# Kernel tuning notes

Measured on AMD Instinct MI355X. Metric: run time of the kernel, lower is better.

Reference implementation:

```python
import jax, jax.numpy as jnp
import numpy as np

L, H, D_IN, D_OUT = 2, 768, 768, 512


def _gru_layer(x, w_ih, w_hh, b_ih, b_hh):
    # x: [B,T,D]; w_ih: [3H,D]; w_hh: [3H,H]; b_ih,b_hh: [3H]
    # PyTorch GRU gate order: r, z, n
    gates_x = jnp.einsum('btd,gd->btg', x, w_ih) + b_ih  # [B,T,3H], precomputed once
    gates_x = jnp.swapaxes(gates_x, 0, 1)  # [T,B,3H] for scan over time
    h0 = jnp.zeros((x.shape[0], w_hh.shape[1]), dtype=x.dtype)

    def step(h, gx):
        gh = h @ w_hh.T + b_hh  # [B,3H]
        xr, xz, xn = jnp.split(gx, 3, axis=-1)
        hr, hz, hn = jnp.split(gh, 3, axis=-1)
        r = jax.nn.sigmoid(xr + hr)
        z = jax.nn.sigmoid(xz + hz)
        n = jnp.tanh(xn + r * hn)
        h_new = (1.0 - z) * n + z * h
        return h_new, h_new

    _, ys = jax.lax.scan(step, h0, gates_x)  # ys: [T,B,H]
    return jnp.swapaxes(ys, 0, 1)  # [B,T,H]


def setup_inputs() -> dict:
    key = jax.random.key(0)
    ks = jax.random.split(key, 6)
    B, T = 16, 1024
    s = 1.0 / np.sqrt(H)  # PyTorch RNN init scale
    x = jax.random.normal(ks[0], (B, T, D_IN), dtype=jnp.float32)
    # stacked per-layer GRU weights (D_IN == H so layer 0 stacks cleanly)
    w_ih = jax.random.uniform(ks[1], (L, 3 * H, H), minval=-s, maxval=s, dtype=jnp.float32)
    w_hh = jax.random.uniform(ks[2], (L, 3 * H, H), minval=-s, maxval=s, dtype=jnp.float32)
    b_ih = jax.random.uniform(ks[3], (L, 3 * H), minval=-s, maxval=s, dtype=jnp.float32)
    b_hh = jax.random.uniform(ks[4], (L, 3 * H), minval=-s, maxval=s, dtype=jnp.float32)
    w_fc = jax.random.normal(ks[5], (D_OUT, H), dtype=jnp.float32) * 0.02
    b_fc = jnp.zeros((D_OUT,), dtype=jnp.float32)
    return {"x": x, "w_ih": w_ih, "w_hh": w_hh, "b_ih": b_ih, "b_hh": b_hh,
            "w_fc": w_fc, "b_fc": b_fc}


def reference(x, w_ih, w_hh, b_ih, b_hh, w_fc, b_fc):
    out = x
    for l in range(L):  # small fixed layer loop
        out = _gru_layer(out, w_ih[l], w_hh[l], b_ih[l], b_hh[l])
    out = jnp.einsum('bth,oh->bto', out, w_fc) + b_fc  # Linear(768->512)
    return jax.nn.gelu(out, approximate=False)  # torch gelu (exact)
```

## Files before the change

### kernel.cpp

```cpp
#include <hip/hip_runtime.h>
#include <hip/hip_bf16.h>

#define H     768
#define G3    2304
#define BATCH 16
#define TLEN  1024
#define DOUT  512
#define SLICE 32
#define WPG   24
#define NSCAN 96
#define NFC   64
#define NWG   160
#define NTHR  384

typedef __attribute__((ext_vector_type(8))) short short8;
typedef __attribute__((ext_vector_type(4))) float f32x4;
typedef __attribute__((ext_vector_type(4))) unsigned int u32x4;

union U8 { short8 s; unsigned u[4]; unsigned long long q[2]; };

__device__ __forceinline__ float b2f(ushort u) {
  union { unsigned int ui; float f; } v; v.ui = ((unsigned int)u) << 16; return v.f;
}
__device__ __forceinline__ ushort f2b(float f) {
  union { float f; unsigned int ui; } v; v.f = f;
  unsigned int u = v.ui;
  return (ushort)((u + 0x7fffu + ((u >> 16) & 1u)) >> 16);
}

__device__ __forceinline__ unsigned long long agent_ld64(const void* p) {
  return __hip_atomic_load((const unsigned long long*)p, __ATOMIC_RELAXED, __HIP_MEMORY_SCOPE_AGENT);
}
__device__ __forceinline__ unsigned agent_ld32(const void* p) {
  return __hip_atomic_load((const unsigned*)p, __ATOMIC_RELAXED, __HIP_MEMORY_SCOPE_AGENT);
}
__device__ __forceinline__ void agent_st32(void* p, unsigned v) {
  __hip_atomic_store((unsigned*)p, v, __ATOMIC_RELAXED, __HIP_MEMORY_SCOPE_AGENT);
}
__device__ __forceinline__ void agent_st64(void* p, unsigned long long v) {
  __hip_atomic_store((unsigned long long*)p, v, __ATOMIC_RELAXED, __HIP_MEMORY_SCOPE_AGENT);
}

__device__ __forceinline__ void ld64B_agent(const void* p, u32x4* r) {
  asm volatile(
    "global_load_dwordx4 %0, %4, off sc0 sc1\n\t"
    "global_load_dwordx4 %1, %4, off offset:16 sc0 sc1\n\t"
    "global_load_dwordx4 %2, %4, off offset:32 sc0 sc1\n\t"
    "global_load_dwordx4 %3, %4, off offset:48 sc0 sc1\n\t"
    "s_waitcnt vmcnt(0)"
    : "=&v"(r[0]), "=&v"(r[1]), "=&v"(r[2]), "=&v"(r[3])
    : "v"(p) : "memory");
}

__device__ __forceinline__ short8 loadA8(const void* base, bool bf, size_t eidx) {
  if (bf) return *(const short8*)((const ushort*)base + eidx);
  const uint4* f = (const uint4*)((const float*)base + eidx);
  uint4 lo = f[0];
  uint4 hi = f[1];
  U8 r;
  r.u[0] = __builtin_amdgcn_perm(lo.y, lo.x, 0x07060302);
  r.u[1] = __builtin_amdgcn_perm(lo.w, lo.z, 0x07060302);
  r.u[2] = __builtin_amdgcn_perm(hi.y, hi.x, 0x07060302);
  r.u[3] = __builtin_amdgcn_perm(hi.w, hi.z, 0x07060302);
  return r.s;
}
__device__ __forceinline__ short8 loadW8(const void* base, bool bf, size_t eidx) {
  if (bf) return *(const short8*)((const ushort*)base + eidx);
  const float* f = (const float*)base + eidx;
  short8 r;
  #pragma unroll
  for (int i = 0; i < 8; i++) r[i] = (short)f2b(f[i]);
  return r;
}
__device__ __forceinline__ float loadS(const void* p, bool bf, size_t i) {
  return bf ? b2f(((const ushort*)p)[i]) : ((const float*)p)[i];
}

__device__ __forceinline__ bool detect_bf16(const unsigned* xw, int tid, int nthr, int* sh) {
  if (tid == 0) *sh = 0;
  __syncthreads();
  int c = 0;
  for (int i = tid; i < 4096; i += nthr) {
    int e = (int)((xw[i] >> 7) & 0xFF);
    c += (e >= 110 && e <= 140) ? 1 : 0;
  }
  atomicAdd(sh, c);
  __syncthreads();
  return *sh > 2048;
}

__device__ __forceinline__ unsigned* flagp(unsigned* flags, int grp, int wgi, int rep) {
  return flags + (((grp * WPG + wgi) * 4 + rep) * 32);
}

__global__ __launch_bounds__(NTHR) void scan_kernel(
    const void* __restrict__ x,
    const void* __restrict__ w_ih,
    const void* __restrict__ w_hh,
    const void* __restrict__ b_ih,
    const void* __restrict__ b_hh,
    const void* __restrict__ w_fc,
    const void* __restrict__ b_fc,
    unsigned int* flags,
    ushort* h1buf,
    float*  gxbuf1,
    float*  gxbuf2,
    ushort* y2,
    void* __restrict__ out)
{
  const int wg   = blockIdx.x;
  const int tid  = threadIdx.x;
  const int wave = tid >> 6;
  const int lane = tid & 63;
  const int quad = lane >> 4;

  __shared__ ushort h_lds[BATCH * H];
  __shared__ float ghs[96 * 17];
  __shared__ float hold[BATCH * SLICE];
  __shared__ float bih_s[96], bhh_s[96];
  __shared__ unsigned donecnt[2];
  __shared__ int   detsh;

  const bool isbf = detect_bf16((const unsigned*)x, tid, NTHR, &detsh);

  if (wg >= NSCAN) {
    const int fcw = wg - NSCAN;
    const unsigned* fpoll = (wave == 0 && lane < WPG)
        ? flagp(flags, 3, lane, (fcw < 32) ? 2 : 3) : nullptr;
    const int sb  = tid / 24;
    const int seg = tid % 24;
    const int sx  = sb & 7;
    const int ar  = lane & 15;
    const int arx = ar & 7;

    for (int i = 0; i < 16; i++) {
      const int t = fcw + 64 * i;
      if (wave == 0) {
        const int tgt = t + 5;
        for (;;) {
          int v = fpoll ? (int)agent_ld32(fpoll) : 0x7FFFFFFF;
          if (__ballot(v < tgt) == 0ull) break;
          __builtin_amdgcn_s_sleep(8);
        }
      }
      __syncthreads();

      {
        const ushort* src = y2 + ((size_t)sb * TLEN + t) * H + seg * 32;
        u32x4 r4[4];
        ld64B_agent(src, r4);
        #pragma unroll
        for (int j = 0; j < 4; j++)
          *(u32x4*)&h_lds[sb * H + (((seg * 4 + j) ^ sx) * 8)] = r4[j];
      }
      __syncthreads();

      if (wave < 4) {
        const int n0 = wave * 128;
        const ushort* abase = &h_lds[ar * H];
        f32x4 acc[8];
        #pragma unroll
        for (int nt = 0; nt < 8; nt++) acc[nt] = (f32x4){0.f, 0.f, 0.f, 0.f};
        for (int kk = 0; kk < 12; kk++) {
          short8 a0 = *(const short8*)&abase[((quad + 4 * kk) ^ arx) * 8];
          short8 a1 = *(const short8*)&abase[((quad + 4 * (kk + 12)) ^ arx) * 8];
          #pragma unroll
          for (int nt = 0; nt < 8; nt++) {
            const size_t bb = (size_t)(n0 + nt * 16 + ar) * H + quad * 8;
            short8 b0 = loadA8(w_fc, isbf, bb + kk * 32);
            short8 b1 = loadA8(w_fc, isbf, bb + (kk + 12) * 32);
            acc[nt] = __builtin_amdgcn_mfma_f32_16x16x32_bf16(a0, b0, acc[nt], 0, 0, 0);
            acc[nt] = __builtin_amdgcn_mfma_f32_16x16x32_bf16(a1, b1, acc[nt], 0, 0, 0);
          }
        }
        #pragma unroll
        for (int nt = 0; nt < 8; nt++) {
          #pragma unroll
          for (int i2 = 0; i2 < 4; i2++) {
            const int b = quad * 4 + i2;
            const int n = n0 + nt * 16 + ar;
            float v = acc[nt][i2] + loadS(b_fc, isbf, n);
            float g = 0.5f * v * (1.0f + erff(v * 0.70710678118654752f));
            if (isbf) ((ushort*)out)[((size_t)b * TLEN + t) * DOUT + n] = f2b(g);
            else      ((float*)out)[((size_t)b * TLEN + t) * DOUT + n] = g;
          }
        }
      }
      __syncthreads();
    }
    return;
  }

  const int grp  = wg / WPG;
  const int wgi  = wg % WPG;
  const bool isL = (grp == 1 || grp == 3);

  if (tid < 2) donecnt[tid] = 0u;
  for (int i = tid; i < BATCH * SLICE; i += NTHR) hold[i] = 0.0f;

  if (isL) {
    size_t boff = (grp == 3) ? (size_t)G3 : 0;
    for (int gf = tid; gf < 96; gf += NTHR) {
      size_t gidx = boff + (size_t)(gf >> 5) * H + wgi * SLICE + (gf & 31);
      bih_s[gf] = loadS(b_ih, isbf, gidx);
      bhh_s[gf] = loadS(b_hh, isbf, gidx);
    }
  }

  const unsigned* pollp = nullptr;
  int polloff = 0;
  if (wave == 0) {
    if (grp == 0) {
      if (lane == 0) { pollp = flagp(flags, 1, wgi, 2); polloff = -2; }
    } else if (grp == 1) {
      if      (lane == 0)  { pollp = flagp(flags, 0, wgi, 0);       polloff = 0;  }
      else if (lane <= 24) { pollp = flagp(flags, 1, lane - 1, 0);  polloff = 0;  }
      else if (lane <= 48) { pollp = flagp(flags, 2, lane - 25, 0); polloff = -2; }
    } else if (grp == 2) {
      if      (lane < 24)  { pollp = flagp(flags, 1, lane, 1);      polloff = 0;  }
      else if (lane == 24) { pollp = flagp(flags, 3, wgi, 1);       polloff = -1; }
    } else {
      if      (lane == 0)  { pollp = flagp(flags, 2, wgi, 1);       polloff = -1; }
      else if (lane <= 24) { pollp = flagp(flags, 3, lane - 1, 0);  polloff = 0;  }
    }
  }

  const void* Wmat = (grp == 0 || grp == 2) ? w_ih : w_hh;
  const size_t woff = (grp >= 2) ? (size_t)G3 * H : 0;
  const int gate   = wave >> 1;
  const int gfbase = gate * SLICE + (wave & 1) * 16;
  const int nrow   = gate * H + wgi * SLICE + (wave & 1) * 16 + (lane & 15);
  const size_t wbase = woff + (size_t)nrow * H + quad * 8;

  short8 bfrag[24];
  #pragma unroll
  for (int kk = 0; kk < 24; kk++)
    bfrag[kk] = loadW8(Wmat, isbf, wbase + kk * 32);

  const int sb  = tid / 24;
  const int seg = tid % 24;
  const int sx  = sb & 7;

  const int pb = tid >> 4;
  const int pj = (tid & 15) * 2;
  const bool pact = isL && (tid < BATCH * SLICE / 2);

  const int lag = (grp == 1) ? 1 : ((grp == 2) ? 2 : ((grp == 3) ? 4 : 0));

  __syncthreads();

  for (int t = 0; t < TLEN + 4; t++) {
    const int tau = t - lag;
    const bool active = (tau >= 0) && (tau < TLEN);

    if (active) {
      if (wave == 0) {
        for (;;) {
          int v = pollp ? (int)agent_ld32(pollp) : 0x7FFFFFFF;
          if (__ballot(v < t + polloff) == 0ull) break;
          __builtin_amdgcn_s_sleep(1);
        }
      }
      __syncthreads();

      unsigned long long gr01 = 0, gz01 = 0, gn01 = 0;
      if (pact) {
        const float* gxr = ((grp == 1) ? gxbuf1 : gxbuf2)
            + ((size_t)((tau & 3) * WPG + wgi) * BATCH + pb) * 96;
        gr01 = agent_ld64(gxr + pj);
        gz01 = agent_ld64(gxr + 32 + pj);
        gn01 = agent_ld64(gxr + 64 + pj);
      }

      if (grp == 0) {
        const size_t srcbase = ((size_t)sb * TLEN + tau) * H + seg * 32;
        #pragma unroll
        for (int i = 0; i < 4; i++) {
          short8 v = loadA8(x, isbf, srcbase + i * 8);
          *(short8*)&h_lds[sb * H + (((seg * 4 + i) ^ sx) * 8)] = v;
        }
      } else {
        const int hstep = (grp == 3) ? (t - 5) : (t - 2);
        u32x4 r4[4];
        if (hstep >= 0) {
          const ushort* src = (grp == 3)
              ? y2 + ((size_t)sb * TLEN + hstep) * H + seg * 32
              : h1buf + (size_t)(hstep & 3) * (BATCH * H) + (size_t)sb * H + seg * 32;
          ld64B_agent(src, r4);
        } else {
          r4[0] = (u32x4){0u, 0u, 0u, 0u};
          r4[1] = r4[0]; r4[2] = r4[0]; r4[3] = r4[0];
        }
        #pragma unroll
        for (int j = 0; j < 4; j++)
          *(u32x4*)&h_lds[sb * H + (((seg * 4 + j) ^ sx) * 8)] = r4[j];
      }
      __syncthreads();

      const int ar  = lane & 15;
      const int arx = ar & 7;
      const ushort* abase = &h_lds[ar * H];
      f32x4 acc0 = {0.f, 0.f, 0.f, 0.f}, acc1 = {0.f, 0.f, 0.f, 0.f};
      #pragma unroll
      for (int kk = 0; kk < 12; kk++) {
        short8 a0 = *(const short8*)&abase[((quad + 4 * kk) ^ arx) * 8];
        short8 a1 = *(const short8*)&abase[((quad + 4 * (kk + 12)) ^ arx) * 8];
        acc0 = __builtin_amdgcn_mfma_f32_16x16x32_bf16(a0, bfrag[kk],      acc0, 0, 0, 0);
        acc1 = __builtin_amdgcn_mfma_f32_16x16x32_bf16(a1, bfrag[kk + 12], acc1, 0, 0, 0);
      }
      f32x4 acc = acc0 + acc1;

      #pragma unroll
      for (int i = 0; i < 4; i++)
        ghs[(gfbase + ar) * 17 + quad * 4 + i] = acc[i];
      __syncthreads();

      if (!isL) {
        float* gxout = ((grp == 0) ? gxbuf1 : gxbuf2)
            + ((size_t)(tau & 3) * WPG + wgi) * BATCH * 96;
        const int m  = tid / 24;
        const int c4 = (tid % 24) * 4;
        union { unsigned long long q; float f[2]; } p0, p1;
        p0.f[0] = ghs[(c4 + 0) * 17 + m];
        p0.f[1] = ghs[(c4 + 1) * 17 + m];
        p1.f[0] = ghs[(c4 + 2) * 17 + m];
        p1.f[1] = ghs[(c4 + 3) * 17 + m];
        agent_st64(gxout + (size_t)m * 96 + c4,     p0.q);
        agent_st64(gxout + (size_t)m * 96 + c4 + 2, p1.q);
      } else if (pact) {
        union { unsigned long long q; float f[2]; } ur, uz, un;
        ur.q = gr01; uz.q = gz01; un.q = gn01;
        unsigned hpack = 0;
        #pragma unroll
        for (int s = 0; s < 2; s++) {
          const int j = pj + s;
          float rpre = ur.f[s] + bih_s[j]      + ghs[j * 17 + pb]        + bhh_s[j];
          float zpre = uz.f[s] + bih_s[32 + j] + ghs[(32 + j) * 17 + pb] + bhh_s[32 + j];
          float hn   = ghs[(64 + j) * 17 + pb] + bhh_s[64 + j];
          float r = 1.0f / (1.0f + expf(-rpre));
          float z = 1.0f / (1.0f + expf(-zpre));
          float n = tanhf(un.f[s] + bih_s[64 + j] + r * hn);
          float hnew = (1.0f - z) * n + z * hold[pb * SLICE + j];
          hold[pb * SLICE + j] = hnew;
          hpack |= ((unsigned)f2b(hnew)) << (16 * s);
        }
        if (grp == 1)
          agent_st32(h1buf + (size_t)(tau & 3) * (BATCH * H)
                           + (size_t)pb * H + wgi * SLICE + pj, hpack);
        else
          agent_st32(&y2[((size_t)pb * TLEN + tau) * H + wgi * SLICE + pj], hpack);

        asm volatile("s_waitcnt vmcnt(0)" ::: "memory");
        if ((tid & 63) == 0) {
          unsigned prev = atomicAdd(&donecnt[t & 1], 1u);
          if (prev == 3u) {
            donecnt[t & 1] = 0u;
            #pragma unroll
            for (int r = 0; r < 4; r++)
              agent_st32(flagp(flags, grp, wgi, r), (unsigned)(t + 1));
          }
        }
      }
    }

    __syncthreads();
    if (tid < 4 && (!isL || !active))
      agent_st32(flagp(flags, grp, wgi, tid), (unsigned)(t + 1));
  }
}

extern "C" void kernel_launch(void* const* d_in, const int* in_sizes, int n_in,
                              void* d_out, int out_size, void* d_ws, size_t ws_size,
                              hipStream_t stream) {
  const void* x    = d_in[0];
  const void* w_ih = d_in[1];
  const void* w_hh = d_in[2];
  const void* b_ih = d_in[3];
  const void* b_hh = d_in[4];
  const void* w_fc = d_in[5];
  const void* b_fc = d_in[6];

  char* ws = (char*)d_ws;
  unsigned int* flags = (unsigned int*)(ws);
  ushort* h1buf  = (ushort*)(ws + 53248);
  float*  gxbuf1 = (float*)(ws + 151552);
  float*  gxbuf2 = (float*)(ws + 741376);
  ushort* y2     = (ushort*)(ws + 1331200);

  hipMemsetAsync(ws, 0, 49152, stream);
  scan_kernel<<<dim3(NWG), dim3(NTHR), 0, stream>>>(
      x, w_ih, w_hh, b_ih, b_hh, w_fc, b_fc, flags,
      h1buf, gxbuf1, gxbuf2, y2, d_out);
}
```

Baseline: 3.965 ms.

## Co-locate recurrent GRU workgroups on one XCD and sync through local L2

Launches extra workgroups, reads each block's XCC id from a hardware register, and has block 0 assign roles so that each recurrent group's 24 workgroups sit on a single XCD where possible. Those clustered groups exchange hidden state and step flags through XCD-local L2 (sc0 loads, workgroup-scope stores) instead of device-coherent memory, aiming to cut per-timestep synchronization latency on the serial scan. A timeout falls back to the device-coherent path, and the state is still written to global buffers for consumers on other XCDs. This adds a startup rendezvous, relies on placement and cache-coherence assumptions, and spare workgroups exit immediately.

```diff
diff --git a/kernel.cpp b/kernel.cpp
--- a/kernel.cpp
+++ b/kernel.cpp
@@ -8,10 +8,9 @@
 #define DOUT  512
 #define SLICE 32
 #define WPG   24
-#define NSCAN 96
-#define NFC   64
-#define NWG   160
+#define NWG   256
 #define NTHR  384
+#define TMO   4096
 
 typedef __attribute__((ext_vector_type(8))) short short8;
 typedef __attribute__((ext_vector_type(4))) float f32x4;
@@ -39,6 +38,16 @@
 }
 __device__ __forceinline__ void agent_st64(void* p, unsigned long long v) {
   __hip_atomic_store((unsigned long long*)p, v, __ATOMIC_RELAXED, __HIP_MEMORY_SCOPE_AGENT);
+}
+
+__device__ __forceinline__ void l2_st32(void* p, unsigned v) {
+  __hip_atomic_store((unsigned*)p, v, __ATOMIC_RELAXED, __HIP_MEMORY_SCOPE_WORKGROUP);
+}
+__device__ __forceinline__ unsigned l2_ld32(const void* p) {
+  unsigned v;
+  asm volatile("global_load_dword %0, %1, off sc0\n\ts_waitcnt vmcnt(0)"
+               : "=v"(v) : "v"(p) : "memory");
+  return v;
 }
 
 __device__ __forceinline__ void ld64B_agent(const void* p, u32x4* r) {
@@ -47,6 +56,16 @@
     "global_load_dwordx4 %1, %4, off offset:16 sc0 sc1\n\t"
     "global_load_dwordx4 %2, %4, off offset:32 sc0 sc1\n\t"
     "global_load_dwordx4 %3, %4, off offset:48 sc0 sc1\n\t"
+    "s_waitcnt vmcnt(0)"
+    : "=&v"(r[0]), "=&v"(r[1]), "=&v"(r[2]), "=&v"(r[3])
+    : "v"(p) : "memory");
+}
+__device__ __forceinline__ void ld64B_sc0(const void* p, u32x4* r) {
+  asm volatile(
+    "global_load_dwordx4 %0, %4, off sc0\n\t"
+    "global_load_dwordx4 %1, %4, off offset:16 sc0\n\t"
+    "global_load_dwordx4 %2, %4, off offset:32 sc0\n\t"
+    "global_load_dwordx4 %3, %4, off offset:48 sc0\n\t"
     "s_waitcnt vmcnt(0)"
     : "=&v"(r[0]), "=&v"(r[1]), "=&v"(r[2]), "=&v"(r[3])
     : "v"(p) : "memory");
@@ -102,13 +121,16 @@
     const void* __restrict__ w_fc,
     const void* __restrict__ b_fc,
     unsigned int* flags,
+    unsigned int* reg,
+    unsigned int* asg,
     ushort* h1buf,
+    ushort* h1L,
+    ushort* y2L,
     float*  gxbuf1,
     float*  gxbuf2,
     ushort* y2,
     void* __restrict__ out)
 {
-  const int wg   = blockIdx.x;
   const int tid  = threadIdx.x;
   const int wave = tid >> 6;
   const int lane = tid & 63;
@@ -119,12 +141,72 @@
   __shared__ float hold[BATCH * SLICE];
   __shared__ float bih_s[96], bhh_s[96];
   __shared__ unsigned donecnt[2];
-  __shared__ int   detsh;
+  __shared__ unsigned cxA[NWG];
+  __shared__ unsigned caA[NWG];
+  __shared__ unsigned masg;
+  __shared__ int fbsh;
+  __shared__ int detsh;
 
   const bool isbf = detect_bf16((const unsigned*)x, tid, NTHR, &detsh);
 
-  if (wg >= NSCAN) {
-    const int fcw = wg - NSCAN;
+  unsigned xcc = __builtin_amdgcn_s_getreg(20 | (3 << 11)) & 7u;
+  if (tid == 0) agent_st32(&reg[blockIdx.x], xcc | 8u);
+  if (blockIdx.x == 0) {
+    for (int i = tid; i < NWG; i += NTHR) {
+      unsigned v;
+      while ((v = agent_ld32(&reg[i])) == 0u) __builtin_amdgcn_s_sleep(8);
+      cxA[i] = v & 7u;
+    }
+    __syncthreads();
+    if (tid == 0) {
+      int cnt[8];
+      for (int i = 0; i < 8; i++) cnt[i] = 0;
+      for (int i = 0; i < NWG; i++) { caA[i] = 0u; cnt[cxA[i]]++; }
+      int xa = 0;
+      for (int x2 = 1; x2 < 8; x2++) if (cnt[x2] > cnt[xa]) xa = x2;
+      int got = 0;
+      for (int i = 0; i < NWG && got < WPG; i++)
+        if (!caA[i] && (int)cxA[i] == xa) {
+          caA[i] = 1u | (1u << 1) | ((unsigned)got << 4) | 0x400u;
+          cnt[xa]--; got++;
+        }
+      int xb = 0;
+      for (int x2 = 1; x2 < 8; x2++) if (cnt[x2] > cnt[xb]) xb = x2;
+      const unsigned cl3 = (cnt[xb] >= WPG) ? 0x400u : 0u;
+      got = 0;
+      for (int i = 0; i < NWG && got < WPG; i++) {
+        if (caA[i]) continue;
+        if (cl3 && (int)cxA[i] != xb) continue;
+        caA[i] = 1u | (3u << 1) | ((unsigned)got << 4) | cl3;
+        got++;
+      }
+      const int gcnt[3] = {WPG, WPG, 64};
+      const unsigned ggrp[3] = {0u, 2u, 4u};
+      for (int k = 0; k < 3; k++) {
+        got = 0;
+        for (int i = 0; i < NWG && got < gcnt[k]; i++)
+          if (!caA[i]) { caA[i] = 1u | (ggrp[k] << 1) | ((unsigned)got << 4); got++; }
+      }
+      for (int i = 0; i < NWG; i++) if (!caA[i]) caA[i] = 0x8000u;
+    }
+    __syncthreads();
+    for (int i = tid; i < NWG; i += NTHR) agent_st32(&asg[i], caA[i]);
+  }
+  if (tid == 0) {
+    unsigned v;
+    while ((v = agent_ld32(&asg[blockIdx.x])) == 0u) __builtin_amdgcn_s_sleep(8);
+    masg = v;
+  }
+  __syncthreads();
+  const unsigned a = masg;
+  if (a == 0x8000u) return;
+  const int grp  = (int)((a >> 1) & 7u);
+  const int wgi  = (int)((a >> 4) & 63u);
+  const bool clu = (a & 0x400u) != 0u;
+  const bool isL = (grp == 1 || grp == 3);
+
+  if (grp == 4) {
+    const int fcw = wgi;
     const unsigned* fpoll = (wave == 0 && lane < WPG)
         ? flagp(flags, 3, lane, (fcw < 32) ? 2 : 3) : nullptr;
     const int sb  = tid / 24;
@@ -191,11 +273,8 @@
     return;
   }
 
-  const int grp  = wg / WPG;
-  const int wgi  = wg % WPG;
-  const bool isL = (grp == 1 || grp == 3);
-
   if (tid < 2) donecnt[tid] = 0u;
+  if (tid == 0) fbsh = 0;
   for (int i = tid; i < BATCH * SLICE; i += NTHR) hold[i] = 0.0f;
 
   if (isL) {
@@ -207,21 +286,27 @@
     }
   }
 
-  const unsigned* pollp = nullptr;
+  const unsigned* pollA = nullptr;
+  const unsigned* pollF = nullptr;
   int polloff = 0;
+  bool ploc = false;
   if (wave == 0) {
     if (grp == 0) {
-      if (lane == 0) { pollp = flagp(flags, 1, wgi, 2); polloff = -2; }
+      if (lane == 0) { pollA = pollF = flagp(flags, 1, wgi, 2); polloff = -2; }
     } else if (grp == 1) {
-      if      (lane == 0)  { pollp = flagp(flags, 0, wgi, 0);       polloff = 0;  }
-      else if (lane <= 24) { pollp = flagp(flags, 1, lane - 1, 0);  polloff = 0;  }
-      else if (lane <= 48) { pollp = flagp(flags, 2, lane - 25, 0); polloff = -2; }
+      if      (lane == 0)  { pollA = pollF = flagp(flags, 0, wgi, 0); polloff = 0; }
+      else if (lane <= 24) { pollA = flagp(flags, 1, lane - 1, 0);
+                             pollF = flagp(flags, 1, lane - 1, 1);
+                             polloff = 0; ploc = clu; }
+      else if (lane <= 48) { pollA = pollF = flagp(flags, 2, lane - 25, 0); polloff = -2; }
     } else if (grp == 2) {
-      if      (lane < 24)  { pollp = flagp(flags, 1, lane, 1);      polloff = 0;  }
-      else if (lane == 24) { pollp = flagp(flags, 3, wgi, 1);       polloff = -1; }
+      if      (lane < 24)  { pollA = pollF = flagp(flags, 1, lane, 1); polloff = 0; }
+      else if (lane == 24) { pollA = pollF = flagp(flags, 3, wgi, 1);  polloff = -1; }
     } else {
-      if      (lane == 0)  { pollp = flagp(flags, 2, wgi, 1);       polloff = -1; }
-      else if (lane <= 24) { pollp = flagp(flags, 3, lane - 1, 0);  polloff = 0;  }
+      if      (lane == 0)  { pollA = pollF = flagp(flags, 2, wgi, 1);  polloff = -1; }
+      else if (lane <= 24) { pollA = flagp(flags, 3, lane - 1, 0);
+                             pollF = flagp(flags, 3, lane - 1, 1);
+                             polloff = 0; ploc = clu; }
     }
   }
 
@@ -247,6 +332,8 @@
 
   const int lag = (grp == 1) ? 1 : ((grp == 2) ? 2 : ((grp == 3) ? 4 : 0));
 
+  bool fb = false;
+
   __syncthreads();
 
   for (int t = 0; t < TLEN + 4; t++) {
@@ -255,13 +342,17 @@
 
     if (active) {
       if (wave == 0) {
+        int iter = 0;
         for (;;) {
-          int v = pollp ? (int)agent_ld32(pollp) : 0x7FFFFFFF;
+          int v = 0x7FFFFFFF;
+          if (pollA) v = (ploc && !fb) ? (int)l2_ld32(pollA) : (int)agent_ld32(pollF);
           if (__ballot(v < t + polloff) == 0ull) break;
+          if (ploc && !fb && ++iter > TMO) { fb = true; fbsh = 1; }
           __builtin_amdgcn_s_sleep(1);
         }
       }
       __syncthreads();
+      const bool useloc = clu && (fbsh == 0);
 
       unsigned long long gr01 = 0, gz01 = 0, gn01 = 0;
       if (pact) {
@@ -283,10 +374,24 @@
         const int hstep = (grp == 3) ? (t - 5) : (t - 2);
         u32x4 r4[4];
         if (hstep >= 0) {
-          const ushort* src = (grp == 3)
-              ? y2 + ((size_t)sb * TLEN + hstep) * H + seg * 32
-              : h1buf + (size_t)(hstep & 3) * (BATCH * H) + (size_t)sb * H + seg * 32;
-          ld64B_agent(src, r4);
+          if (grp == 2) {
+            const ushort* src = h1buf + (size_t)(hstep & 3) * (BATCH * H)
+                                      + (size_t)sb * H + seg * 32;
+            ld64B_agent(src, r4);
+          } else if (grp == 1) {
+            const ushort* src = (useloc ? h1L : h1buf)
+                + (size_t)(hstep & 3) * (BATCH * H) + (size_t)sb * H + seg * 32;
+            if (useloc) ld64B_sc0(src, r4); else ld64B_agent(src, r4);
+          } else {
+            if (useloc) {
+              const ushort* src = y2L + (size_t)(hstep & 3) * (BATCH * H)
+                                      + (size_t)sb * H + seg * 32;
+              ld64B_sc0(src, r4);
+            } else {
+              const ushort* src = y2 + ((size_t)sb * TLEN + hstep) * H + seg * 32;
+              ld64B_agent(src, r4);
+            }
+          }
         } else {
           r4[0] = (u32x4){0u, 0u, 0u, 0u};
           r4[1] = r4[0]; r4[2] = r4[0]; r4[3] = r4[0];
@@ -344,28 +449,33 @@
           hold[pb * SLICE + j] = hnew;
           hpack |= ((unsigned)f2b(hnew)) << (16 * s);
         }
+        const size_t soff = (size_t)(tau & 3) * (BATCH * H)
+                          + (size_t)pb * H + wgi * SLICE + pj;
+        if (clu) {
+          l2_st32(((grp == 1) ? h1L : y2L) + soff, hpack);
+          asm volatile("s_waitcnt vmcnt(0)" ::: "memory");
+          if ((tid & 63) == 0) {
+            unsigned prev = atomicAdd(&donecnt[t & 1], 1u);
+            if (prev == 3u) {
+              donecnt[t & 1] = 0u;
+              l2_st32(flagp(flags, grp, wgi, 0), (unsigned)(t + 1));
+            }
+          }
+        }
         if (grp == 1)
-          agent_st32(h1buf + (size_t)(tau & 3) * (BATCH * H)
-                           + (size_t)pb * H + wgi * SLICE + pj, hpack);
+          agent_st32(h1buf + soff, hpack);
         else
           agent_st32(&y2[((size_t)pb * TLEN + tau) * H + wgi * SLICE + pj], hpack);
-
-        asm volatile("s_waitcnt vmcnt(0)" ::: "memory");
-        if ((tid & 63) == 0) {
-          unsigned prev = atomicAdd(&donecnt[t & 1], 1u);
-          if (prev == 3u) {
-            donecnt[t & 1] = 0u;
-            #pragma unroll
-            for (int r = 0; r < 4; r++)
-              agent_st32(flagp(flags, grp, wgi, r), (unsigned)(t + 1));
-          }
-        }
       }
     }
 
     __syncthreads();
-    if (tid < 4 && (!isL || !active))
+    if (tid >= 1 && tid < 4)
       agent_st32(flagp(flags, grp, wgi, tid), (unsigned)(t + 1));
+    if (tid == 0 && !(isL && active && clu)) {
+      if (isL && clu) l2_st32(flagp(flags, grp, wgi, 0), (unsigned)(t + 1));
+      else            agent_st32(flagp(flags, grp, wgi, 0), (unsigned)(t + 1));
+    }
   }
 }
 
@@ -382,13 +492,17 @@
 
   char* ws = (char*)d_ws;
   unsigned int* flags = (unsigned int*)(ws);
+  unsigned int* reg   = (unsigned int*)(ws + 49152);
+  unsigned int* asg   = (unsigned int*)(ws + 50176);
   ushort* h1buf  = (ushort*)(ws + 53248);
   float*  gxbuf1 = (float*)(ws + 151552);
   float*  gxbuf2 = (float*)(ws + 741376);
-  ushort* y2     = (ushort*)(ws + 1331200);
-
-  hipMemsetAsync(ws, 0, 49152, stream);
+  ushort* h1L    = (ushort*)(ws + 1331200);
+  ushort* y2L    = (ushort*)(ws + 1429504);
+  ushort* y2     = (ushort*)(ws + 1527808);
+
+  hipMemsetAsync(ws, 0, 51200, stream);
   scan_kernel<<<dim3(NWG), dim3(NTHR), 0, stream>>>(
-      x, w_ih, w_hh, b_ih, b_hh, w_fc, b_fc, flags,
-      h1buf, gxbuf1, gxbuf2, y2, d_out);
-}
+      x, w_ih, w_hh, b_ih, b_hh, w_fc, b_fc, flags, reg, asg,
+      h1buf, h1L, y2L, gxbuf1, gxbuf2, y2, d_out);
+}
```

New measurement: 5.293 ms. +33.5%, slower.
